# Kernel tuning notes

Hardware: AMD Instinct MI355X
Metric: run time of the kernel (lower is better)

The kernel has to match this reference:

```python
import jax, jax.numpy as jnp
import numpy as np

B = 524288  # batch of hand configurations

# Fixed ShadowHand tree topology: 28 nodes, 23 joints.
PARENTS = np.array([-1, 0, 1, 2, 3, 4, 0, 6, 7, 8, 9, 0, 11, 12, 13, 14,
                    0, 16, 17, 18, 19, 20, 0, 22, 23, 24, 25, 26])
# joint index attached at each node (-1 for fingertips, which are pure translations)
NODE_JOINT = np.array([0, 1, 2, 3, 4, -1, 5, 6, 7, 8, -1, 9, 10, 11, 12, -1,
                       13, 14, 15, 16, 17, -1, 18, 19, 20, 21, 22, -1])
KEYPOINTS = [0, 22, 25, 26, 27, 1, 3, 4, 5, 6, 8, 9, 10, 11, 13, 14, 15, 17, 19, 20, 21]

TRANSLATION = np.array([
    [0.0, 0.0, 0.0], [0.033, 0.0, 0.095], [0.0, 0.0, 0.0], [0.0, 0.0, 0.045], [0.0, 0.0, 0.025], [0.0, 0.0, 0.026],
    [0.011, 0.0, 0.099], [0.0, 0.0, 0.0], [0.0, 0.0, 0.045], [0.0, 0.0, 0.025], [0.0, 0.0, 0.026],
    [-0.011, 0.0, 0.095], [0.0, 0.0, 0.0], [0.0, 0.0, 0.045], [0.0, 0.0, 0.025], [0.0, 0.0, 0.026],
    [-0.017, 0.0, 0.044], [-0.017, 0.0, 0.044], [0.0, 0.0, 0.0], [0.0, 0.0, 0.045], [0.0, 0.0, 0.025], [0.0, 0.0, 0.026],
    [0.034, -0.009, 0.029], [0.0, 0.0, 0.0], [0.0, 0.0, 0.038], [0.0, 0.0, 0.0], [0.0, 0.0, 0.032], [0.0, 0.0, 0.0275],
], dtype=np.float32)

AXES = np.array([
    [1.0, 0.0, 0.0], [0.0, 1.0, 0.0], [1.0, 0.0, 0.0], [1.0, 0.0, 0.0], [1.0, 0.0, 0.0],
    [0.0, 1.0, 0.0], [1.0, 0.0, 0.0], [1.0, 0.0, 0.0], [1.0, 0.0, 0.0],
    [0.0, 1.0, 0.0], [1.0, 0.0, 0.0], [1.0, 0.0, 0.0], [1.0, 0.0, 0.0],
    [0.571, 0.0, 0.821], [0.0, 1.0, 0.0], [1.0, 0.0, 0.0], [1.0, 0.0, 0.0], [1.0, 0.0, 0.0],
    [0.0, 0.0, -1.0], [1.0, 0.0, 0.0], [1.0, 0.0, 0.0], [0.0, 1.0, 0.0], [0.0, 1.0, 0.0],
], dtype=np.float32)

MIN_RAD = np.array([-0.689, -0.349, 0.0, 0.0, 0.0, -0.349, 0.0, 0.0, 0.0, -0.349, 0.0, 0.0, 0.0,
                    0.0, -0.349, 0.0, 0.0, 0.0, -1.047, 0.0, -0.209, -0.524, -1.571], dtype=np.float32)
MAX_RAD = np.array([0.489, 0.349, 1.571, 1.571, 1.571, 0.349, 1.571, 1.571, 1.571, 0.349, 1.571, 1.571, 1.571,
                    0.785, 0.349, 1.571, 1.571, 1.571, 1.047, 1.222, 0.209, 0.524, 0.0], dtype=np.float32)


def setup_inputs() -> dict:
    key = jax.random.key(0)
    angles = jax.random.normal(key, (B, 23), dtype=jnp.float32)
    return {
        "angles": angles,
        "axes": jnp.asarray(AXES),
        "min_rad": jnp.asarray(MIN_RAD),
        "max_rad": jnp.asarray(MAX_RAD),
        "translation": jnp.asarray(TRANSLATION),
    }


def _hat(x):
    # x: [..., 3] -> skew-symmetric [..., 3, 3]
    x0, x1, x2 = x[..., 0], x[..., 1], x[..., 2]
    z = jnp.zeros_like(x0)
    return jnp.stack([
        jnp.stack([z, -x2, x1], axis=-1),
        jnp.stack([x2, z, -x0], axis=-1),
        jnp.stack([-x1, x0, z], axis=-1),
    ], axis=-2)


def _fk(angles, axes, min_rad, max_rad, translation):
    a = jnp.clip(angles, min_rad, max_rad)            # [B, 23]
    H = _hat(axes)                                    # [23, 3, 3]
    HH = jnp.matmul(H, H)                             # [23, 3, 3]
    s = jnp.sin(a)[..., None, None]                   # [B, 23, 1, 1]
    c = jnp.cos(a)[..., None, None]
    eye = jnp.eye(3, dtype=angles.dtype)
    R = eye + s * H + (1.0 - c) * HH                  # [B, 23, 3, 3] (Rodrigues)

    Rw = [None] * 28
    tw = [None] * 28
    Rw[0] = R[:, 0]                                   # palm joint WR0
    tw[0] = jnp.broadcast_to(translation[0], angles.shape[:-1] + (3,))
    # fixed small tree traversal (27 steps), parents always precede children
    for n in range(1, 28):
        p = int(PARENTS[n])
        j = int(NODE_JOINT[n])
        tw[n] = tw[p] + jnp.einsum('bij,j->bi', Rw[p], translation[n])
        if j >= 0:
            Rw[n] = jnp.matmul(Rw[p], R[:, j])
    return jnp.stack([tw[k] for k in KEYPOINTS], axis=-2)  # [B, 21, 3]


def reference(angles, axes, min_rad, max_rad, translation):
    return _fk(angles, axes, min_rad, max_rad, translation)
```

## Files before the change

### kernel.cpp

```cpp
#include <hip/hip_runtime.h>

namespace {

constexpr int TPB = 64;

__device__ __forceinline__ float clampf(float x, float lo, float hi) {
  return fminf(fmaxf(x, lo), hi);
}


__global__ __launch_bounds__(TPB, 5) void fk_kernel(
    const float* __restrict__ angles,
    float* __restrict__ out) {
  __shared__ float lds[32 * 63];

  const int tid = threadIdx.x;
  const long long base = (long long)blockIdx.x * TPB;

  {
    const float4* __restrict__ src = reinterpret_cast<const float4*>(angles + base * 23);
    float4* dst = reinterpret_cast<float4*>(lds);
#pragma unroll
    for (int k = 0; k < 6; ++k) {
      int idx = tid + k * TPB;
      if (idx < (TPB * 23) / 4) dst[idx] = src[idx];
    }
  }
  __syncthreads();

  const float* al = lds + tid * 23;

  float o[63];

  const float a0 = clampf(al[0], -0.689f, 0.489f);
  const float s0 = __sinf(a0);
  const float c0 = __cosf(a0);

  o[0] = 0.0f; o[1] = 0.0f; o[2] = 0.0f;

#define FINGER(TX, TZ, JY, LOY, RB)                                             \
  {                                                                             \
    const float aY = clampf(al[(JY)], (LOY), -(LOY));                           \
    const float sY = __sinf(aY), cY = __cosf(aY);                               \
    const float g1 = clampf(al[(JY) + 1], 0.0f, 1.571f);                        \
    const float g2 = g1 + clampf(al[(JY) + 2], 0.0f, 1.571f);                   \
    const float g3 = g2 + clampf(al[(JY) + 3], 0.0f, 1.571f);                   \
    const float s1 = __sinf(g1), c1 = __cosf(g1);                               \
    const float s2 = __sinf(g2), c2 = __cosf(g2);                               \
    const float s3 = __sinf(g3), c3 = __cosf(g3);                               \
    const float t1x = (TX), t1y = -s0 * (TZ), t1z = c0 * (TZ);                  \
    o[3 * (RB) + 0] = t1x; o[3 * (RB) + 1] = t1y; o[3 * (RB) + 2] = t1z;        \
    const float vx = sY, vy = -s0 * cY, vz = c0 * cY;           \
                                                  \
    const float q3y = -0.045f * s1, q3z = 0.045f * c1;                          \
    const float q4y = q3y - 0.025f * s2, q4z = q3z + 0.025f * c2;               \
    const float q5y = q4y - 0.026f * s3, q5z = q4z + 0.026f * c3;               \
    o[3 * ((RB) + 1) + 0] = t1x + q3z * vx;                                     \
    o[3 * ((RB) + 1) + 1] = t1y + q3y * c0 + q3z * vy;                          \
    o[3 * ((RB) + 1) + 2] = t1z + q3y * s0 + q3z * vz;                          \
    o[3 * ((RB) + 2) + 0] = t1x + q4z * vx;                                     \
    o[3 * ((RB) + 2) + 1] = t1y + q4y * c0 + q4z * vy;                          \
    o[3 * ((RB) + 2) + 2] = t1z + q4y * s0 + q4z * vz;                          \
    o[3 * ((RB) + 3) + 0] = t1x + q5z * vx;                                     \
    o[3 * ((RB) + 3) + 1] = t1y + q5y * c0 + q5z * vy;                          \
    o[3 * ((RB) + 3) + 2] = t1z + q5y * s0 + q5z * vz;                          \
  }

  FINGER(0.033f, 0.095f, 1, -0.349f, 5)
  FINGER(0.011f, 0.099f, 5, -0.349f, 9)
  FINGER(-0.011f, 0.095f, 9, -0.349f, 13)
#undef FINGER

  {
    const float a13 = clampf(al[13], 0.0f, 0.785f);
    const float wx = 0.571f, wz = 0.821f;
    const float s13 = __sinf(a13), c13 = __cosf(a13);
    const float t13 = 1.0f - c13;
    const float g00 = 1.0f - t13 * (wz * wz), g10 = s13 * wz, g20 = t13 * (wx * wz);
    const float g01 = -s13 * wz, g11 = 1.0f - t13 * (wx * wx + wz * wz), g21 = s13 * wx;
    const float g02 = t13 * (wx * wz), g12 = -s13 * wx, g22 = 1.0f - t13 * (wx * wx);
    const float gdx = -0.017f * g00 + 0.044f * g02;
    const float gdy = -0.017f * g10 + 0.044f * g12;
    const float gdz = -0.017f * g20 + 0.044f * g22;
    const float t17x = -0.017f + gdx;
    const float t17y = -0.044f * s0 + (c0 * gdy - s0 * gdz);
    const float t17z = 0.044f * c0 + (s0 * gdy + c0 * gdz);
    o[51] = t17x; o[52] = t17y; o[53] = t17z;
    const float a14 = clampf(al[14], -0.349f, 0.349f);
    const float s14 = __sinf(a14), c14 = __cosf(a14);
    const float ux = g01, uy = c0 * g11 - s0 * g21, uz = s0 * g11 + c0 * g21;
    const float mx = s14 * g00 + c14 * g02;
    const float my = s14 * g10 + c14 * g12;
    const float mz = s14 * g20 + c14 * g22;
    const float vx = mx, vy = c0 * my - s0 * mz, vz = s0 * my + c0 * mz;
    const float g1 = clampf(al[15], 0.0f, 1.571f);
    const float g2 = g1 + clampf(al[16], 0.0f, 1.571f);
    const float g3 = g2 + clampf(al[17], 0.0f, 1.571f);
    const float s1 = __sinf(g1), c1 = __cosf(g1);
    const float s2 = __sinf(g2), c2 = __cosf(g2);
    const float s3 = __sinf(g3), c3 = __cosf(g3);
    const float q3y = -0.045f * s1, q3z = 0.045f * c1;
    const float q4y = q3y - 0.025f * s2, q4z = q3z + 0.025f * c2;
    const float q5y = q4y - 0.026f * s3, q5z = q4z + 0.026f * c3;
    o[54] = t17x + q3y * ux + q3z * vx;
    o[55] = t17y + q3y * uy + q3z * vy;
    o[56] = t17z + q3y * uz + q3z * vz;
    o[57] = t17x + q4y * ux + q4z * vx;
    o[58] = t17y + q4y * uy + q4z * vy;
    o[59] = t17z + q4y * uz + q4z * vz;
    o[60] = t17x + q5y * ux + q5z * vx;
    o[61] = t17y + q5y * uy + q5z * vy;
    o[62] = t17z + q5y * uz + q5z * vz;
  }

  {
    const float a18 = clampf(al[18], -1.047f, 1.047f);
    const float s18 = __sinf(a18), c18 = __cosf(a18);
    const float t22x = 0.034f;
    const float t22y = -0.009f * c0 - 0.029f * s0;
    const float t22z = -0.009f * s0 + 0.029f * c0;
    o[3] = t22x; o[4] = t22y; o[5] = t22z;
    const float a19 = clampf(al[19], 0.0f, 1.222f);
    const float a20 = clampf(al[20], -0.209f, 0.209f);
    const float a21 = clampf(al[21], -0.524f, 0.524f);
    const float a22 = clampf(al[22], -1.571f, 0.0f);
    const float s19 = __sinf(a19), c19 = __cosf(a19);
    const float sg = a19 + a20;
    const float ss = __sinf(sg), cs = __cosf(sg);
    const float s21 = __sinf(a21), c21 = __cosf(a21);
    const float ta = a21 + a22;
    const float st = __sinf(ta), ct = __cosf(ta);
    const float qAy = -0.038f * s19, qAz = 0.038f * c19;
    const float q6x = 0.032f * s21;
    const float q6y = qAy - 0.032f * c21 * ss;
    const float q6z = qAz + 0.032f * c21 * cs;
    const float q7x = q6x + 0.0275f * st;
    const float q7y = q6y - 0.0275f * ct * ss;
    const float q7z = q6z + 0.0275f * ct * cs;
    const float m10 = c0 * s18, m11 = c0 * c18, m20 = s0 * s18, m21 = s0 * c18;
    o[6] = t22x + qAy * s18;
    o[7] = t22y + qAy * m11 - qAz * s0;
    o[8] = t22z + qAy * m21 + qAz * c0;
    o[9] = t22x + q6x * c18 + q6y * s18;
    o[10] = t22y - q6x * m10 + q6y * m11 - q6z * s0;
    o[11] = t22z - q6x * m20 + q6y * m21 + q6z * c0;
    o[12] = t22x + q7x * c18 + q7y * s18;
    o[13] = t22y - q7x * m10 + q7y * m11 - q7z * s0;
    o[14] = t22z - q7x * m20 + q7y * m21 + q7z * c0;
  }

  __syncthreads();

#pragma unroll
  for (int p = 0; p < 2; ++p) {
    if ((tid >> 5) == p) {
      float* dst = lds + (tid & 31) * 63;
#pragma unroll
      for (int k = 0; k < 63; ++k) dst[k] = o[k];
    }
    __syncthreads();
    const float4* lsrc = reinterpret_cast<const float4*>(lds);
    float4* gdst = reinterpret_cast<float4*>(out + (base + 32 * p) * 63);
#pragma unroll
    for (int it = 0; it < 8; ++it) {
      int idx = tid + it * TPB;
      if (idx < (32 * 63) / 4) gdst[idx] = lsrc[idx];
    }
    __syncthreads();
  }
}

}

extern "C" void kernel_launch(void* const* d_in, const int* in_sizes, int n_in,
                              void* d_out, int out_size, void* d_ws, size_t ws_size,
                              hipStream_t stream) {
  const float* angles = (const float*)d_in[0];
  float* out = (float*)d_out;
  const int Bn = in_sizes[0] / 23;
  const int nblocks = Bn / TPB;
  fk_kernel<<<nblocks, TPB, 0, stream>>>(angles, out);
}
```

Baseline: 33.16 us.

## Split per-sample finger chains across four wavefronts per 64-sample block

Each block now handles 64 samples with 256 threads, and each of four wavefronts computes a different subset of finger chains for the same sample. Work per thread and the output array shrink from 63 to at most 24 floats, which lowers register pressure and allows a single full-size LDS staging pass instead of two half passes. The cost is that every wave redundantly computes the palm rotation, the wave-level branches give uneven per-wave work (wave 1 does two fingers), and more threads are launched.

```diff
diff --git a/kernel.cpp b/kernel.cpp
--- a/kernel.cpp
+++ b/kernel.cpp
@@ -2,76 +2,74 @@
 
 namespace {
 
-constexpr int TPB = 64;
+constexpr int TPB = 256;
+constexpr int EPB = 64;
 
 __device__ __forceinline__ float clampf(float x, float lo, float hi) {
   return fminf(fmaxf(x, lo), hi);
 }
 
 
-__global__ __launch_bounds__(TPB, 5) void fk_kernel(
+__global__ __launch_bounds__(TPB, 8) void fk_kernel(
     const float* __restrict__ angles,
     float* __restrict__ out) {
-  __shared__ float lds[32 * 63];
+  __shared__ float lds[EPB * 63];
 
   const int tid = threadIdx.x;
-  const long long base = (long long)blockIdx.x * TPB;
+  const int lane = tid & 63;
+  const int w = tid >> 6;
+  const long long base = (long long)blockIdx.x * EPB;
 
   {
     const float4* __restrict__ src = reinterpret_cast<const float4*>(angles + base * 23);
     float4* dst = reinterpret_cast<float4*>(lds);
-#pragma unroll
-    for (int k = 0; k < 6; ++k) {
-      int idx = tid + k * TPB;
-      if (idx < (TPB * 23) / 4) dst[idx] = src[idx];
-    }
+    dst[tid] = src[tid];
+    if (tid + TPB < (EPB * 23) / 4) dst[tid + TPB] = src[tid + TPB];
   }
   __syncthreads();
 
-  const float* al = lds + tid * 23;
-
-  float o[63];
+  const float* al = lds + lane * 23;
+  float o[24];
 
   const float a0 = clampf(al[0], -0.689f, 0.489f);
   const float s0 = __sinf(a0);
   const float c0 = __cosf(a0);
 
-  o[0] = 0.0f; o[1] = 0.0f; o[2] = 0.0f;
-
-#define FINGER(TX, TZ, JY, LOY, RB)                                             \
+#define FINGER(TX, TZ, J, OB)                                                   \
   {                                                                             \
-    const float aY = clampf(al[(JY)], (LOY), -(LOY));                           \
+    const float aY = clampf(al[(J)], -0.349f, 0.349f);                          \
     const float sY = __sinf(aY), cY = __cosf(aY);                               \
-    const float g1 = clampf(al[(JY) + 1], 0.0f, 1.571f);                        \
-    const float g2 = g1 + clampf(al[(JY) + 2], 0.0f, 1.571f);                   \
-    const float g3 = g2 + clampf(al[(JY) + 3], 0.0f, 1.571f);                   \
+    const float g1 = clampf(al[(J) + 1], 0.0f, 1.571f);                         \
+    const float g2 = g1 + clampf(al[(J) + 2], 0.0f, 1.571f);                    \
+    const float g3 = g2 + clampf(al[(J) + 3], 0.0f, 1.571f);                    \
     const float s1 = __sinf(g1), c1 = __cosf(g1);                               \
     const float s2 = __sinf(g2), c2 = __cosf(g2);                               \
     const float s3 = __sinf(g3), c3 = __cosf(g3);                               \
     const float t1x = (TX), t1y = -s0 * (TZ), t1z = c0 * (TZ);                  \
-    o[3 * (RB) + 0] = t1x; o[3 * (RB) + 1] = t1y; o[3 * (RB) + 2] = t1z;        \
     const float vx = sY, vy = -s0 * cY, vz = c0 * cY;           \
                                                   \
     const float q3y = -0.045f * s1, q3z = 0.045f * c1;                          \
     const float q4y = q3y - 0.025f * s2, q4z = q3z + 0.025f * c2;               \
     const float q5y = q4y - 0.026f * s3, q5z = q4z + 0.026f * c3;               \
-    o[3 * ((RB) + 1) + 0] = t1x + q3z * vx;                                     \
-    o[3 * ((RB) + 1) + 1] = t1y + q3y * c0 + q3z * vy;                          \
-    o[3 * ((RB) + 1) + 2] = t1z + q3y * s0 + q3z * vz;                          \
-    o[3 * ((RB) + 2) + 0] = t1x + q4z * vx;                                     \
-    o[3 * ((RB) + 2) + 1] = t1y + q4y * c0 + q4z * vy;                          \
-    o[3 * ((RB) + 2) + 2] = t1z + q4y * s0 + q4z * vz;                          \
-    o[3 * ((RB) + 3) + 0] = t1x + q5z * vx;                                     \
-    o[3 * ((RB) + 3) + 1] = t1y + q5y * c0 + q5z * vy;                          \
-    o[3 * ((RB) + 3) + 2] = t1z + q5y * s0 + q5z * vz;                          \
+    o[(OB) + 0] = t1x; o[(OB) + 1] = t1y; o[(OB) + 2] = t1z;                    \
+    o[(OB) + 3] = t1x + q3z * vx;                                               \
+    o[(OB) + 4] = t1y + q3y * c0 + q3z * vy;                                    \
+    o[(OB) + 5] = t1z + q3y * s0 + q3z * vz;                                    \
+    o[(OB) + 6] = t1x + q4z * vx;                                               \
+    o[(OB) + 7] = t1y + q4y * c0 + q4z * vy;                                    \
+    o[(OB) + 8] = t1z + q4y * s0 + q4z * vz;                                    \
+    o[(OB) + 9] = t1x + q5z * vx;                                               \
+    o[(OB) + 10] = t1y + q5y * c0 + q5z * vy;                                   \
+    o[(OB) + 11] = t1z + q5y * s0 + q5z * vz;                                   \
   }
 
-  FINGER(0.033f, 0.095f, 1, -0.349f, 5)
-  FINGER(0.011f, 0.099f, 5, -0.349f, 9)
-  FINGER(-0.011f, 0.095f, 9, -0.349f, 13)
-#undef FINGER
-
-  {
+  if (w == 0) {
+    o[0] = 0.0f; o[1] = 0.0f; o[2] = 0.0f;
+    FINGER(0.033f, 0.095f, 1, 3)
+  } else if (w == 1) {
+    FINGER(0.011f, 0.099f, 5, 0)
+    FINGER(-0.011f, 0.095f, 9, 12)
+  } else if (w == 2) {
     const float a13 = clampf(al[13], 0.0f, 0.785f);
     const float wx = 0.571f, wz = 0.821f;
     const float s13 = __sinf(a13), c13 = __cosf(a13);
@@ -85,7 +83,7 @@
     const float t17x = -0.017f + gdx;
     const float t17y = -0.044f * s0 + (c0 * gdy - s0 * gdz);
     const float t17z = 0.044f * c0 + (s0 * gdy + c0 * gdz);
-    o[51] = t17x; o[52] = t17y; o[53] = t17z;
+    o[0] = t17x; o[1] = t17y; o[2] = t17z;
     const float a14 = clampf(al[14], -0.349f, 0.349f);
     const float s14 = __sinf(a14), c14 = __cosf(a14);
     const float ux = g01, uy = c0 * g11 - s0 * g21, uz = s0 * g11 + c0 * g21;
@@ -102,24 +100,22 @@
     const float q3y = -0.045f * s1, q3z = 0.045f * c1;
     const float q4y = q3y - 0.025f * s2, q4z = q3z + 0.025f * c2;
     const float q5y = q4y - 0.026f * s3, q5z = q4z + 0.026f * c3;
-    o[54] = t17x + q3y * ux + q3z * vx;
-    o[55] = t17y + q3y * uy + q3z * vy;
-    o[56] = t17z + q3y * uz + q3z * vz;
-    o[57] = t17x + q4y * ux + q4z * vx;
-    o[58] = t17y + q4y * uy + q4z * vy;
-    o[59] = t17z + q4y * uz + q4z * vz;
-    o[60] = t17x + q5y * ux + q5z * vx;
-    o[61] = t17y + q5y * uy + q5z * vy;
-    o[62] = t17z + q5y * uz + q5z * vz;
-  }
-
-  {
+    o[3] = t17x + q3y * ux + q3z * vx;
+    o[4] = t17y + q3y * uy + q3z * vy;
+    o[5] = t17z + q3y * uz + q3z * vz;
+    o[6] = t17x + q4y * ux + q4z * vx;
+    o[7] = t17y + q4y * uy + q4z * vy;
+    o[8] = t17z + q4y * uz + q4z * vz;
+    o[9] = t17x + q5y * ux + q5z * vx;
+    o[10] = t17y + q5y * uy + q5z * vy;
+    o[11] = t17z + q5y * uz + q5z * vz;
+  } else {
     const float a18 = clampf(al[18], -1.047f, 1.047f);
     const float s18 = __sinf(a18), c18 = __cosf(a18);
     const float t22x = 0.034f;
     const float t22y = -0.009f * c0 - 0.029f * s0;
     const float t22z = -0.009f * s0 + 0.029f * c0;
-    o[3] = t22x; o[4] = t22y; o[5] = t22z;
+    o[0] = t22x; o[1] = t22y; o[2] = t22z;
     const float a19 = clampf(al[19], 0.0f, 1.222f);
     const float a20 = clampf(al[20], -0.209f, 0.209f);
     const float a21 = clampf(al[21], -0.524f, 0.524f);
@@ -138,35 +134,47 @@
     const float q7y = q6y - 0.0275f * ct * ss;
     const float q7z = q6z + 0.0275f * ct * cs;
     const float m10 = c0 * s18, m11 = c0 * c18, m20 = s0 * s18, m21 = s0 * c18;
-    o[6] = t22x + qAy * s18;
-    o[7] = t22y + qAy * m11 - qAz * s0;
-    o[8] = t22z + qAy * m21 + qAz * c0;
-    o[9] = t22x + q6x * c18 + q6y * s18;
-    o[10] = t22y - q6x * m10 + q6y * m11 - q6z * s0;
-    o[11] = t22z - q6x * m20 + q6y * m21 + q6z * c0;
-    o[12] = t22x + q7x * c18 + q7y * s18;
-    o[13] = t22y - q7x * m10 + q7y * m11 - q7z * s0;
-    o[14] = t22z - q7x * m20 + q7y * m21 + q7z * c0;
+    o[3] = t22x + qAy * s18;
+    o[4] = t22y + qAy * m11 - qAz * s0;
+    o[5] = t22z + qAy * m21 + qAz * c0;
+    o[6] = t22x + q6x * c18 + q6y * s18;
+    o[7] = t22y - q6x * m10 + q6y * m11 - q6z * s0;
+    o[8] = t22z - q6x * m20 + q6y * m21 + q6z * c0;
+    o[9] = t22x + q7x * c18 + q7y * s18;
+    o[10] = t22y - q7x * m10 + q7y * m11 - q7z * s0;
+    o[11] = t22z - q7x * m20 + q7y * m21 + q7z * c0;
   }
+#undef FINGER
 
   __syncthreads();
 
+  {
+    float* row = lds + lane * 63;
+    if (w == 0) {
+      row[0] = o[0]; row[1] = o[1]; row[2] = o[2];
 #pragma unroll
-  for (int p = 0; p < 2; ++p) {
-    if ((tid >> 5) == p) {
-      float* dst = lds + (tid & 31) * 63;
+      for (int k = 0; k < 12; ++k) row[15 + k] = o[3 + k];
+    } else if (w == 1) {
 #pragma unroll
-      for (int k = 0; k < 63; ++k) dst[k] = o[k];
+      for (int k = 0; k < 24; ++k) row[27 + k] = o[k];
+    } else if (w == 2) {
+#pragma unroll
+      for (int k = 0; k < 12; ++k) row[51 + k] = o[k];
+    } else {
+#pragma unroll
+      for (int k = 0; k < 12; ++k) row[3 + k] = o[k];
     }
-    __syncthreads();
+  }
+  __syncthreads();
+
+  {
     const float4* lsrc = reinterpret_cast<const float4*>(lds);
-    float4* gdst = reinterpret_cast<float4*>(out + (base + 32 * p) * 63);
+    float4* gdst = reinterpret_cast<float4*>(out + base * 63);
 #pragma unroll
-    for (int it = 0; it < 8; ++it) {
-      int idx = tid + it * TPB;
-      if (idx < (32 * 63) / 4) gdst[idx] = lsrc[idx];
+    for (int k = 0; k < 4; ++k) {
+      int idx = tid + k * TPB;
+      if (idx < (EPB * 63) / 4) gdst[idx] = lsrc[idx];
     }
-    __syncthreads();
   }
 }
 
@@ -178,6 +186,6 @@
   const float* angles = (const float*)d_in[0];
   float* out = (float*)d_out;
   const int Bn = in_sizes[0] / 23;
-  const int nblocks = Bn / TPB;
+  const int nblocks = Bn / EPB;
   fk_kernel<<<nblocks, TPB, 0, stream>>>(angles, out);
 }
```

Result: no change. 33.05 us (median of 2 runs) (-0.3%).
